# Optimization experiments

Measured on AMD Instinct MI355X. Metric: run time of the kernel, lower is better.

The kernel has to match this reference:

```python
import jax, jax.numpy as jnp
import numpy as np
from jax import lax

TAU = 1.0  # registered buffer, default 1.0 -> Q_tau = +inf -> clamp is a no-op
EPS = 1e-5
SQRT2 = float(np.sqrt(2.0))

# sign with straight-through estimator (weights): grad = identity
@jax.custom_vjp
def sign_w(w):
    return jnp.sign(w)
def _sign_w_fwd(w):
    return jnp.sign(w), None
def _sign_w_bwd(_, g):
    return (g,)
sign_w.defvjp(_sign_w_fwd, _sign_w_bwd)

@jax.custom_vjp
def sign_a(x):
    return jnp.sign(x)
def _sign_a_fwd(x):
    return jnp.sign(x), x
def _sign_a_bwd(x, g):
    return (jnp.maximum(2.0 - jnp.abs(2.0 * x), 0.0) * g,)
sign_a.defvjp(_sign_a_fwd, _sign_a_bwd)

def binarize_conv2d(a, w, alpha, stride=1):
    # weight standardization (torch.var is unbiased -> ddof=1)
    w0 = w - jnp.mean(w, axis=(1, 2, 3), keepdims=True)
    var = jnp.var(w0, axis=(1, 2, 3), keepdims=True, ddof=1)
    w1 = w0 * (2.0 * SQRT2) / jnp.sqrt(var + EPS)
    EW = jnp.mean(jnp.abs(w1))
    Q_tau = lax.stop_gradient(-EW * jnp.log(2.0 - 2.0 * TAU))  # +inf for tau=1
    w2 = jnp.clip(w1, -Q_tau, Q_tau)
    bw = sign_w(w2)
    ba = sign_a(a)  # eval mode: a0 = a (no per-sample var normalization)
    out = lax.conv_general_dilated(
        ba, bw, window_strides=(stride, stride), padding=((1, 1), (1, 1)),
        dimension_numbers=('NCHW', 'OIHW', 'NCHW'))
    return out * alpha[None]  # alpha: [C_out,1,1] -> broadcast over N,H,W

def bn_eval(x, gamma, beta, mean, var):
    scale = (gamma / jnp.sqrt(var + EPS)).reshape(1, -1, 1, 1)
    shift = (beta - mean * gamma / jnp.sqrt(var + EPS)).reshape(1, -1, 1, 1)
    return x * scale + shift

def hardtanh(x):
    return jnp.clip(x, -1.0, 1.0)

def setup_inputs() -> dict:
    key = jax.random.key(0)
    ks = jax.random.split(key, 13)
    N, C, H, W = 64, 256, 32, 32
    return {
        'x': jax.random.normal(ks[0], (N, C, H, W), jnp.float32),
        'conv1_w': jax.random.normal(ks[1], (C, C, 3, 3), jnp.float32) * 0.05,
        'alpha1': jax.random.uniform(ks[2], (C, 1, 1), jnp.float32),
        'bn1_gamma': jax.random.uniform(ks[3], (C,), jnp.float32) + 0.5,
        'bn1_beta': jax.random.normal(ks[4], (C,), jnp.float32) * 0.1,
        'bn1_mean': jax.random.normal(ks[5], (C,), jnp.float32),
        'bn1_var': jax.random.uniform(ks[6], (C,), jnp.float32) + 0.5,
        'conv2_w': jax.random.normal(ks[7], (C, C, 3, 3), jnp.float32) * 0.05,
        'alpha2': jax.random.uniform(ks[8], (C, 1, 1), jnp.float32),
        'bn2_gamma': jax.random.uniform(ks[9], (C,), jnp.float32) + 0.5,
        'bn2_beta': jax.random.normal(ks[10], (C,), jnp.float32) * 0.1,
        'bn2_mean': jax.random.normal(ks[11], (C,), jnp.float32),
        'bn2_var': jax.random.uniform(ks[12], (C,), jnp.float32) + 0.5,
    }

def reference(x, conv1_w, alpha1, bn1_gamma, bn1_beta, bn1_mean, bn1_var,
              conv2_w, alpha2, bn2_gamma, bn2_beta, bn2_mean, bn2_var):
    out = hardtanh(bn_eval(binarize_conv2d(x, conv1_w, alpha1, stride=1),
                           bn1_gamma, bn1_beta, bn1_mean, bn1_var))
    out = bn_eval(binarize_conv2d(out, conv2_w, alpha2, stride=1),
                  bn2_gamma, bn2_beta, bn2_mean, bn2_var)
    out = out + x  # identity shortcut (stride=1, in_planes==planes)
    return hardtanh(out)
```

## Files before the change

### kernel.cpp

```cpp
#include <hip/hip_runtime.h>
#include <cstdint>
#include <cstddef>

using u32 = unsigned int;
using u64 = unsigned long long;

typedef int v4i  __attribute__((ext_vector_type(4)));
typedef int v16i __attribute__((ext_vector_type(16)));

#define EPSV 1e-5f

__global__ void prep_weights(const float* __restrict__ w1, const float* __restrict__ w2,
                             const float* __restrict__ a1, const float* __restrict__ g1,
                             const float* __restrict__ b1, const float* __restrict__ m1,
                             const float* __restrict__ v1,
                             const float* __restrict__ a2, const float* __restrict__ g2,
                             const float* __restrict__ b2, const float* __restrict__ m2,
                             const float* __restrict__ v2,
                             unsigned char* __restrict__ Wsgn, float4* __restrict__ SC4)
{
    const int co   = blockIdx.x;
    const int conv = blockIdx.y;
    const int c    = threadIdx.x;
    const float* w = conv ? w2 : w1;

    float wv[9];
    const float* wp = w + ((size_t)co * 256 + c) * 9;
    float s = 0.f;
#pragma unroll
    for (int p = 0; p < 9; ++p) { wv[p] = wp[p]; s += wv[p]; }

    __shared__ float red[256];
    red[c] = s;
    __syncthreads();
    for (int off = 128; off > 0; off >>= 1) {
        if (c < off) red[c] += red[c + off];
        __syncthreads();
    }
    const float mean = __fdiv_rn(red[0], 2304.0f);

    unsigned char* wrow = Wsgn + ((size_t)(conv * 256 + co) * 9) * 256;
#pragma unroll
    for (int p = 0; p < 9; ++p)
        wrow[p * 256 + c] = (wv[p] > mean) ? 0x01u : 0xFFu;

    if (c == 0) {
        const float alpha = conv ? a2[co] : a1[co];
        const float gamma = conv ? g2[co] : g1[co];
        const float beta  = conv ? b2[co] : b1[co];
        const float mu    = conv ? m2[co] : m1[co];
        const float var   = conv ? v2[co] : v1[co];
        const float sq    = __fsqrt_rn(__fadd_rn(var, EPSV));
        const float scale = __fdiv_rn(gamma, sq);
        const float shift = __fsub_rn(beta, __fdiv_rn(__fmul_rn(mu, gamma), sq));
        SC4[conv * 256 + co] = make_float4(alpha, scale, shift, 0.f);
    }
}

__global__ void build_bfrag(const unsigned char* __restrict__ Wsgn, uint4* __restrict__ Bf)
{
    const int f    = blockIdx.x;
    const int lane = threadIdx.x;
    const int conv = f / 576;
    const int rem  = f % 576;
    const int g    = rem / 72;
    const int p    = (rem % 72) / 8;
    const int cb   = rem % 8;
    const int co   = g * 32 + (lane & 31);
    const unsigned char* src = Wsgn + ((size_t)(conv * 256 + co) * 9 + p) * 256
                                    + cb * 32 + (lane >> 5) * 16;
    Bf[(size_t)f * 64 + lane] = *(const uint4*)src;
}

__global__ void binarize_x(const float* __restrict__ x, u32* __restrict__ A1)
{
    const int n = blockIdx.x >> 3;
    const int j = blockIdx.x & 7;
    const int p = threadIdx.x;
    const float* xp = x + (((size_t)n * 256 + j * 32) * 1024) + p;
    u32 bits = 0;
#pragma unroll
    for (int k = 0; k < 32; ++k) {
        float v = xp[(size_t)k * 1024];
        bits |= (v > 0.f ? 1u : 0u) << k;
    }
    A1[((size_t)n * 1024 + p) * 8 + j] = bits;
}

__device__ __forceinline__ u32 expand4(u32 x)
{
    u32 r;
    r  = ((x & 1u) ? 0x00000001u : 0x000000FFu);
    r |= ((x & 2u) ? 0x00000100u : 0x0000FF00u);
    r |= ((x & 4u) ? 0x00010000u : 0x00FF0000u);
    r |= ((x & 8u) ? 0x01000000u : 0xFF000000u);
    return r;
}

template<int CONV>
__global__ __launch_bounds__(256, 2)
void conv_mfma(const u32* __restrict__ A_in, const v4i* __restrict__ Bf,
               const float4* __restrict__ SC4, const float* __restrict__ X,
               u32* __restrict__ A_out, float* __restrict__ OUT)
{
    const int n    = blockIdx.x >> 4;
    const int yp   = blockIdx.x & 15;
    const int q    = blockIdx.y;
    const int tid  = threadIdx.x;
    const int wave = tid >> 6;
    const int lane = tid & 63;
    const int y0   = yp * 2;

    __shared__ alignas(16) unsigned char lds[34816];

    for (int s = tid; s < 2176; s += 256) {
        const int r   = s / 544;
        const int rm  = s - r * 544;
        const int xs  = rm >> 4;
        const int c16 = rm & 15;
        const int iy  = y0 - 1 + r;
        const int ix  = xs - 1;
        u32 d0 = 0, d1 = 0, d2 = 0, d3 = 0;
        if ((unsigned)iy < 32u && (unsigned)ix < 32u) {
            const u32 wrd = A_in[((size_t)n * 1024 + iy * 32 + ix) * 8 + (c16 >> 1)];
            const u32 h = (wrd >> ((c16 & 1) * 16)) & 0xFFFFu;
            d0 = expand4(h);
            d1 = expand4(h >> 4);
            d2 = expand4(h >> 8);
            d3 = expand4(h >> 12);
        }
        const u32 off = ((u32)((r * 34 + xs) * 256 + c16 * 16)) ^ ((u32)(xs & 7) << 4);
        *(uint4*)(lds + off) = make_uint4(d0, d1, d2, d3);
    }
    __syncthreads();

    v16i acc0 = {0,0,0,0,0,0,0,0,0,0,0,0,0,0,0,0};
    v16i acc1 = {0,0,0,0,0,0,0,0,0,0,0,0,0,0,0,0};
    const int g = q * 4 + wave;
    const v4i* Bq = Bf + ((size_t)(((CONV == 2) ? 576 : 0) + g * 72)) * 64 + lane;

#pragma unroll
    for (int p = 0; p < 9; ++p) {
        const int dy = p / 3, dx = p % 3;
        const u32 xs  = (u32)(lane & 31) + (u32)dx;
        const u32 swz = (xs & 7u) << 4;
        const u32 raw = (u32)((dy * 34 + xs) * 256) + (u32)((lane >> 5) * 16);
#pragma unroll
        for (int cb = 0; cb < 8; ++cb) {
            const v4i b  = Bq[(p * 8 + cb) * 64];
            const u32 o0 = (raw + (u32)(cb * 32)) ^ swz;
            const v4i a0 = *(const v4i*)(lds + o0);
            const v4i a1 = *(const v4i*)(lds + o0 + 8704);
            acc0 = __builtin_amdgcn_mfma_i32_32x32x32_i8(a0, b, acc0, 0, 0, 0);
            acc1 = __builtin_amdgcn_mfma_i32_32x32x32_i8(a1, b, acc1, 0, 0, 0);
        }
    }

    const float4 sc = SC4[((CONV == 2) ? 256 : 0) + q * 128 + wave * 32 + (lane & 31)];
    const float alpha = sc.x, scale = sc.y, shift = sc.z;

    if (CONV == 1) {
#define EPILOG1(ACC, YY)                                                        \
        _Pragma("unroll")                                                       \
        for (int reg = 0; reg < 16; ++reg) {                                    \
            const int dot = ACC[reg];                                           \
            const float t = __fadd_rn(__fmul_rn(__fmul_rn((float)dot, alpha),   \
                                                scale), shift);                 \
            const u64 m = __ballot(t > 0.f);                                    \
            const int m0 = (reg & 3) + 8 * (reg >> 2);                          \
            if (lane == 0) {                                                    \
                const size_t pbase = (size_t)n * 1024 + (y0 + (YY)) * 32;       \
                A_out[(pbase + m0) * 8 + g]     = (u32)m;                       \
                A_out[(pbase + m0 + 4) * 8 + g] = (u32)(m >> 32);               \
            }                                                                   \
        }
        EPILOG1(acc0, 0)
        EPILOG1(acc1, 1)
#undef EPILOG1
    } else {
        __syncthreads();
        float* ep = (float*)lds;
        const int co_l = wave * 32 + (lane & 31);
#define EPILOG2(ACC, YY)                                                        \
        _Pragma("unroll")                                                       \
        for (int reg = 0; reg < 16; ++reg) {                                    \
            const int dot = ACC[reg];                                           \
            const float t = __fadd_rn(__fmul_rn(__fmul_rn((float)dot, alpha),   \
                                                scale), shift);                 \
            const int xx = (reg & 3) + 8 * (reg >> 2) + 4 * (lane >> 5);        \
            ep[((YY) * 32 + xx) * 128 + co_l] = t;                              \
        }
        EPILOG2(acc0, 0)
        EPILOG2(acc1, 1)
#undef EPILOG2
        __syncthreads();

        const int co = tid & 127, yy = tid >> 7;
        const size_t base = ((size_t)(n * 256 + q * 128 + co)) * 1024 + (y0 + yy) * 32;
#pragma unroll
        for (int x4 = 0; x4 < 32; x4 += 4) {
            float4 r;
            r.x = ep[(yy * 32 + x4 + 0) * 128 + co];
            r.y = ep[(yy * 32 + x4 + 1) * 128 + co];
            r.z = ep[(yy * 32 + x4 + 2) * 128 + co];
            r.w = ep[(yy * 32 + x4 + 3) * 128 + co];
            const float4 xv = *(const float4*)(X + base + x4);
            r.x = fminf(1.0f, fmaxf(-1.0f, __fadd_rn(r.x, xv.x)));
            r.y = fminf(1.0f, fmaxf(-1.0f, __fadd_rn(r.y, xv.y)));
            r.z = fminf(1.0f, fmaxf(-1.0f, __fadd_rn(r.z, xv.z)));
            r.w = fminf(1.0f, fmaxf(-1.0f, __fadd_rn(r.w, xv.w)));
            *(float4*)(OUT + base + x4) = r;
        }
    }
}

extern "C" void kernel_launch(void* const* d_in, const int* in_sizes, int n_in,
                              void* d_out, int out_size, void* d_ws, size_t ws_size,
                              hipStream_t stream)
{
    const float* x   = (const float*)d_in[0];
    const float* w1  = (const float*)d_in[1];
    const float* al1 = (const float*)d_in[2];
    const float* g1  = (const float*)d_in[3];
    const float* b1  = (const float*)d_in[4];
    const float* m1  = (const float*)d_in[5];
    const float* v1  = (const float*)d_in[6];
    const float* w2  = (const float*)d_in[7];
    const float* al2 = (const float*)d_in[8];
    const float* g2  = (const float*)d_in[9];
    const float* b2  = (const float*)d_in[10];
    const float* m2  = (const float*)d_in[11];
    const float* v2  = (const float*)d_in[12];
    float* out = (float*)d_out;

    char* ws = (char*)d_ws;
    float4*        SC4  = (float4*)(ws);
    unsigned char* Wsgn = (unsigned char*)(ws + (64u << 10));
    uint4*         Bf   = (uint4*)(ws + (2u << 20));
    u32*           A1   = (u32*)(ws + (4u << 20));
    u32*           A2   = (u32*)(ws + (6u << 20));
    (void)ws_size; (void)in_sizes; (void)n_in; (void)out_size;

    prep_weights<<<dim3(256, 2), 256, 0, stream>>>(w1, w2, al1, g1, b1, m1, v1,
                                                   al2, g2, b2, m2, v2, Wsgn, SC4);
    build_bfrag<<<dim3(1152), 64, 0, stream>>>(Wsgn, Bf);
    binarize_x<<<dim3(512), 1024, 0, stream>>>(x, A1);
    conv_mfma<1><<<dim3(1024, 2), 256, 0, stream>>>(A1, (const v4i*)Bf, SC4,
                                                    nullptr, A2, nullptr);
    conv_mfma<2><<<dim3(1024, 2), 256, 0, stream>>>(A2, (const v4i*)Bf, SC4,
                                                    x, nullptr, out);
}
```

Measured before the change: 138.0 us.

## Enlarge conv tile to 4 rows × all 256 output channels per block

Each block now computes 4 output rows for all 256 output channels, with each wave owning two 32-channel groups. Every A fragment read from LDS is reused across two B fragments and every B fragment across four rows, giving 8 accumulators per wave instead of 2. The input halo is rebuilt once per block for all channels instead of once per channel half, and the LDS layout drops the XOR swizzle for a channel-major layout. The costs are higher register pressure (launch bounds lowered to 1 block per CU), a larger LDS footprint, a grid of only 512 blocks, and possible LDS bank conflicts from the unswizzled layout.

```diff
diff --git a/kernel.cpp b/kernel.cpp
--- a/kernel.cpp
+++ b/kernel.cpp
@@ -98,28 +98,27 @@
 }
 
 template<int CONV>
-__global__ __launch_bounds__(256, 2)
+__global__ __launch_bounds__(256, 1)
 void conv_mfma(const u32* __restrict__ A_in, const v4i* __restrict__ Bf,
                const float4* __restrict__ SC4, const float* __restrict__ X,
                u32* __restrict__ A_out, float* __restrict__ OUT)
 {
-    const int n    = blockIdx.x >> 4;
-    const int yp   = blockIdx.x & 15;
-    const int q    = blockIdx.y;
+    const int n    = blockIdx.x >> 3;
+    const int yq   = blockIdx.x & 7;
+    const int y0   = yq * 4;
     const int tid  = threadIdx.x;
     const int wave = tid >> 6;
     const int lane = tid & 63;
-    const int y0   = yp * 2;
-
-    __shared__ alignas(16) unsigned char lds[34816];
-
-    for (int s = tid; s < 2176; s += 256) {
-        const int r   = s / 544;
-        const int rm  = s - r * 544;
-        const int xs  = rm >> 4;
-        const int c16 = rm & 15;
-        const int iy  = y0 - 1 + r;
-        const int ix  = xs - 1;
+
+    __shared__ alignas(16) unsigned char lds[52224];
+
+    for (int s = tid; s < 3264; s += 256) {
+        const int xs   = s % 34;
+        const int rest = s / 34;
+        const int r    = rest % 6;
+        const int c16  = rest / 6;
+        const int iy   = y0 - 1 + r;
+        const int ix   = xs - 1;
         u32 d0 = 0, d1 = 0, d2 = 0, d3 = 0;
         if ((unsigned)iy < 32u && (unsigned)ix < 32u) {
             const u32 wrd = A_in[((size_t)n * 1024 + iy * 32 + ix) * 8 + (c16 >> 1)];
@@ -129,88 +128,104 @@
             d2 = expand4(h >> 8);
             d3 = expand4(h >> 12);
         }
-        const u32 off = ((u32)((r * 34 + xs) * 256 + c16 * 16)) ^ ((u32)(xs & 7) << 4);
-        *(uint4*)(lds + off) = make_uint4(d0, d1, d2, d3);
+        *(uint4*)(lds + ((c16 * 6 + r) * 34 + xs) * 16) = make_uint4(d0, d1, d2, d3);
     }
     __syncthreads();
 
-    v16i acc0 = {0,0,0,0,0,0,0,0,0,0,0,0,0,0,0,0};
-    v16i acc1 = {0,0,0,0,0,0,0,0,0,0,0,0,0,0,0,0};
-    const int g = q * 4 + wave;
-    const v4i* Bq = Bf + ((size_t)(((CONV == 2) ? 576 : 0) + g * 72)) * 64 + lane;
+    const v16i Z = {0,0,0,0,0,0,0,0,0,0,0,0,0,0,0,0};
+    v16i acc00 = Z, acc01 = Z, acc10 = Z, acc11 = Z;
+    v16i acc20 = Z, acc21 = Z, acc30 = Z, acc31 = Z;
+
+    const int g0 = wave * 2, g1 = g0 + 1;
+    const v4i* B0 = Bf + ((size_t)(((CONV == 2) ? 576 : 0) + g0 * 72)) * 64 + lane;
+    const v4i* B1 = Bf + ((size_t)(((CONV == 2) ? 576 : 0) + g1 * 72)) * 64 + lane;
+    const u32 labase = (u32)((lane >> 5) * 3264 + (lane & 31) * 16);
 
 #pragma unroll
     for (int p = 0; p < 9; ++p) {
         const int dy = p / 3, dx = p % 3;
-        const u32 xs  = (u32)(lane & 31) + (u32)dx;
-        const u32 swz = (xs & 7u) << 4;
-        const u32 raw = (u32)((dy * 34 + xs) * 256) + (u32)((lane >> 5) * 16);
 #pragma unroll
         for (int cb = 0; cb < 8; ++cb) {
-            const v4i b  = Bq[(p * 8 + cb) * 64];
-            const u32 o0 = (raw + (u32)(cb * 32)) ^ swz;
-            const v4i a0 = *(const v4i*)(lds + o0);
-            const v4i a1 = *(const v4i*)(lds + o0 + 8704);
-            acc0 = __builtin_amdgcn_mfma_i32_32x32x32_i8(a0, b, acc0, 0, 0, 0);
-            acc1 = __builtin_amdgcn_mfma_i32_32x32x32_i8(a1, b, acc1, 0, 0, 0);
+            const v4i b0 = B0[(p * 8 + cb) * 64];
+            const v4i b1 = B1[(p * 8 + cb) * 64];
+            const u32 ob = labase + (u32)(cb * 6528 + dy * 544 + dx * 16);
+            const v4i a0 = *(const v4i*)(lds + ob);
+            const v4i a1 = *(const v4i*)(lds + ob + 544);
+            const v4i a2 = *(const v4i*)(lds + ob + 1088);
+            const v4i a3 = *(const v4i*)(lds + ob + 1632);
+            acc00 = __builtin_amdgcn_mfma_i32_32x32x32_i8(a0, b0, acc00, 0, 0, 0);
+            acc01 = __builtin_amdgcn_mfma_i32_32x32x32_i8(a0, b1, acc01, 0, 0, 0);
+            acc10 = __builtin_amdgcn_mfma_i32_32x32x32_i8(a1, b0, acc10, 0, 0, 0);
+            acc11 = __builtin_amdgcn_mfma_i32_32x32x32_i8(a1, b1, acc11, 0, 0, 0);
+            acc20 = __builtin_amdgcn_mfma_i32_32x32x32_i8(a2, b0, acc20, 0, 0, 0);
+            acc21 = __builtin_amdgcn_mfma_i32_32x32x32_i8(a2, b1, acc21, 0, 0, 0);
+            acc30 = __builtin_amdgcn_mfma_i32_32x32x32_i8(a3, b0, acc30, 0, 0, 0);
+            acc31 = __builtin_amdgcn_mfma_i32_32x32x32_i8(a3, b1, acc31, 0, 0, 0);
         }
     }
 
-    const float4 sc = SC4[((CONV == 2) ? 256 : 0) + q * 128 + wave * 32 + (lane & 31)];
-    const float alpha = sc.x, scale = sc.y, shift = sc.z;
+    const int col = lane & 31;
+    const float4 sc0 = SC4[((CONV == 2) ? 256 : 0) + g0 * 32 + col];
+    const float4 sc1 = SC4[((CONV == 2) ? 256 : 0) + g1 * 32 + col];
 
     if (CONV == 1) {
-#define EPILOG1(ACC, YY)                                                        \
-        _Pragma("unroll")                                                       \
-        for (int reg = 0; reg < 16; ++reg) {                                    \
-            const int dot = ACC[reg];                                           \
-            const float t = __fadd_rn(__fmul_rn(__fmul_rn((float)dot, alpha),   \
-                                                scale), shift);                 \
-            const u64 m = __ballot(t > 0.f);                                    \
-            const int m0 = (reg & 3) + 8 * (reg >> 2);                          \
-            if (lane == 0) {                                                    \
-                const size_t pbase = (size_t)n * 1024 + (y0 + (YY)) * 32;       \
-                A_out[(pbase + m0) * 8 + g]     = (u32)m;                       \
-                A_out[(pbase + m0 + 4) * 8 + g] = (u32)(m >> 32);               \
-            }                                                                   \
-        }
-        EPILOG1(acc0, 0)
-        EPILOG1(acc1, 1)
-#undef EPILOG1
+#define EP1(ACC, RY, G, SC)                                                     \
+        { _Pragma("unroll")                                                     \
+          for (int reg = 0; reg < 16; ++reg) {                                  \
+              const float t = __fadd_rn(__fmul_rn(__fmul_rn((float)ACC[reg],    \
+                                        SC.x), SC.y), SC.z);                    \
+              const u64 m = __ballot(t > 0.f);                                  \
+              if (lane == 0) {                                                  \
+                  const int x = (reg & 3) + 8 * (reg >> 2);                     \
+                  const size_t pb = (size_t)n * 1024 + (y0 + (RY)) * 32 + x;    \
+                  A_out[pb * 8 + (G)]       = (u32)m;                           \
+                  A_out[(pb + 4) * 8 + (G)] = (u32)(m >> 32);                   \
+              } } }
+        EP1(acc00, 0, g0, sc0)  EP1(acc01, 0, g1, sc1)
+        EP1(acc10, 1, g0, sc0)  EP1(acc11, 1, g1, sc1)
+        EP1(acc20, 2, g0, sc0)  EP1(acc21, 2, g1, sc1)
+        EP1(acc30, 3, g0, sc0)  EP1(acc31, 3, g1, sc1)
+#undef EP1
     } else {
         __syncthreads();
         float* ep = (float*)lds;
-        const int co_l = wave * 32 + (lane & 31);
-#define EPILOG2(ACC, YY)                                                        \
-        _Pragma("unroll")                                                       \
-        for (int reg = 0; reg < 16; ++reg) {                                    \
-            const int dot = ACC[reg];                                           \
-            const float t = __fadd_rn(__fmul_rn(__fmul_rn((float)dot, alpha),   \
-                                                scale), shift);                 \
-            const int xx = (reg & 3) + 8 * (reg >> 2) + 4 * (lane >> 5);        \
-            ep[((YY) * 32 + xx) * 128 + co_l] = t;                              \
-        }
-        EPILOG2(acc0, 0)
-        EPILOG2(acc1, 1)
-#undef EPILOG2
-        __syncthreads();
-
-        const int co = tid & 127, yy = tid >> 7;
-        const size_t base = ((size_t)(n * 256 + q * 128 + co)) * 1024 + (y0 + yy) * 32;
-#pragma unroll
-        for (int x4 = 0; x4 < 32; x4 += 4) {
-            float4 r;
-            r.x = ep[(yy * 32 + x4 + 0) * 128 + co];
-            r.y = ep[(yy * 32 + x4 + 1) * 128 + co];
-            r.z = ep[(yy * 32 + x4 + 2) * 128 + co];
-            r.w = ep[(yy * 32 + x4 + 3) * 128 + co];
-            const float4 xv = *(const float4*)(X + base + x4);
-            r.x = fminf(1.0f, fmaxf(-1.0f, __fadd_rn(r.x, xv.x)));
-            r.y = fminf(1.0f, fmaxf(-1.0f, __fadd_rn(r.y, xv.y)));
-            r.z = fminf(1.0f, fmaxf(-1.0f, __fadd_rn(r.z, xv.z)));
-            r.w = fminf(1.0f, fmaxf(-1.0f, __fadd_rn(r.w, xv.w)));
-            *(float4*)(OUT + base + x4) = r;
-        }
+#define EP2PASS(A0, A1, RY)                                                     \
+        { _Pragma("unroll")                                                     \
+          for (int reg = 0; reg < 16; ++reg) {                                  \
+              const int x = (reg & 3) + 8 * (reg >> 2) + 4 * (lane >> 5);       \
+              const float t0 = __fadd_rn(__fmul_rn(__fmul_rn((float)A0[reg],    \
+                                         sc0.x), sc0.y), sc0.z);                \
+              const float t1 = __fadd_rn(__fmul_rn(__fmul_rn((float)A1[reg],    \
+                                         sc1.x), sc1.y), sc1.z);                \
+              ep[x * 257 + g0 * 32 + col] = t0;                                 \
+              ep[x * 257 + g1 * 32 + col] = t1;                                 \
+          }                                                                     \
+          __syncthreads();                                                      \
+          {                                                                     \
+              const int co = tid;                                               \
+              const size_t gb = ((size_t)(n * 256 + co)) * 1024                 \
+                              + (y0 + (RY)) * 32;                               \
+              _Pragma("unroll")                                                 \
+              for (int x4 = 0; x4 < 32; x4 += 4) {                              \
+                  float4 r;                                                     \
+                  r.x = ep[(x4 + 0) * 257 + co];                                \
+                  r.y = ep[(x4 + 1) * 257 + co];                                \
+                  r.z = ep[(x4 + 2) * 257 + co];                                \
+                  r.w = ep[(x4 + 3) * 257 + co];                                \
+                  const float4 xv = *(const float4*)(X + gb + x4);              \
+                  r.x = fminf(1.f, fmaxf(-1.f, __fadd_rn(r.x, xv.x)));          \
+                  r.y = fminf(1.f, fmaxf(-1.f, __fadd_rn(r.y, xv.y)));          \
+                  r.z = fminf(1.f, fmaxf(-1.f, __fadd_rn(r.z, xv.z)));          \
+                  r.w = fminf(1.f, fmaxf(-1.f, __fadd_rn(r.w, xv.w)));          \
+                  *(float4*)(OUT + gb + x4) = r;                                \
+              }                                                                 \
+          }                                                                     \
+          __syncthreads(); }
+        EP2PASS(acc00, acc01, 0)
+        EP2PASS(acc10, acc11, 1)
+        EP2PASS(acc20, acc21, 2)
+        EP2PASS(acc30, acc31, 3)
+#undef EP2PASS
     }
 }
 
@@ -245,8 +260,8 @@
                                                    al2, g2, b2, m2, v2, Wsgn, SC4);
     build_bfrag<<<dim3(1152), 64, 0, stream>>>(Wsgn, Bf);
     binarize_x<<<dim3(512), 1024, 0, stream>>>(x, A1);
-    conv_mfma<1><<<dim3(1024, 2), 256, 0, stream>>>(A1, (const v4i*)Bf, SC4,
-                                                    nullptr, A2, nullptr);
-    conv_mfma<2><<<dim3(1024, 2), 256, 0, stream>>>(A2, (const v4i*)Bf, SC4,
-                                                    x, nullptr, out);
-}
+    conv_mfma<1><<<dim3(512), 256, 0, stream>>>(A1, (const v4i*)Bf, SC4,
+                                                nullptr, A2, nullptr);
+    conv_mfma<2><<<dim3(512), 256, 0, stream>>>(A2, (const v4i*)Bf, SC4,
+                                                x, nullptr, out);
+}
```

Result: slower. 186.8 us (+35.3%).
